# Kernel optimization log

Hardware: AMD Instinct MI355X
Metric: run time of the kernel (lower is better)

The kernel has to match this reference:

```python
import jax, jax.numpy as jnp
import numpy as np
from jax import lax

# dims: T steps, B batch, V vocab, E embed, H hidden, N cache slots, DK key dim, DV value dim
T, B, V, E, H, N, DK, DV = 64, 32, 32000, 512, 512, 512, 256, 512


def setup_inputs() -> dict:
    key = jax.random.key(0)
    ks = jax.random.split(key, 12)
    rn = lambda i, shape, scale: jax.random.normal(ks[i], shape, jnp.float32) * scale
    return {
        "tokens": jax.random.randint(ks[0], (T, B), 0, V),
        "emb": rn(1, (V, E), 0.02),
        "Wq": rn(2, (E, DK), E ** -0.5),
        "Wk": rn(3, (E, DK), E ** -0.5),
        "Wv": rn(4, (H, DV), H ** -0.5),
        "Wh": rn(5, (E + DV, H), (E + DV) ** -0.5),
        "bh": jnp.zeros((H,), jnp.float32),
        "Wout": rn(6, (H, V), H ** -0.5),
        "bout": jnp.zeros((V,), jnp.float32),
        "keys0": rn(7, (N, DK), 0.02),
        "values0": rn(8, (N, DV), 0.02),
        "k": 8,
    }


def reference(tokens, emb, Wq, Wk, Wv, Wh, bh, Wout, bout, keys0, values0, k):
    scale = 1.0 / jnp.sqrt(jnp.float32(DK))

    def step(carry, tok_t):
        keys, vals, ptr = carry
        x = emb[tok_t]                                  # [B, E] embedding gather
        q = x @ Wq                                      # [B, DK]
        scores = (q @ keys.T) * scale                   # [B, N]
        top_s, top_i = lax.top_k(scores, k)             # [B, k]
        w = jax.nn.softmax(top_s, axis=-1)              # [B, k]
        v_sel = vals[top_i]                             # [B, k, DV] irregular gather
        retrieved = jnp.einsum('bk,bkd->bd', w, v_sel)  # [B, DV]
        h = jnp.tanh(jnp.concatenate([x, retrieved], axis=-1) @ Wh + bh)  # [B, H]
        # circular-pointer cache write (batch-pooled key/value)
        new_key = jnp.mean(x @ Wk, axis=0)              # [DK]
        new_val = jnp.mean(h @ Wv, axis=0)              # [DV]
        keys = lax.dynamic_update_slice(keys, new_key[None, :], (ptr, 0))
        vals = lax.dynamic_update_slice(vals, new_val[None, :], (ptr, 0))
        ptr = (ptr + 1) % N
        return (keys, vals, ptr), h

    init = (keys0, values0, jnp.int32(0))
    _, hiddens = lax.scan(step, init, tokens)           # [T, B, H]
    logits = hiddens @ Wout + bout                      # [T, B, V]
    return logits
```

## Files before the change

kernel.cpp:

```cpp
#include <hip/hip_runtime.h>

typedef _Float16 half_t;
typedef _Float16 half8 __attribute__((ext_vector_type(8)));
typedef float f32x4 __attribute__((ext_vector_type(4)));


__device__ __forceinline__ void gload_lds16(const void* g, void* l) {
  __builtin_amdgcn_global_load_lds((const __attribute__((address_space(1))) void*)g,
                                   (__attribute__((address_space(3))) void*)l, 16, 0, 0);
}

__device__ __forceinline__ void prepTile(int pid, const float* __restrict__ Wout,
                                         half_t* __restrict__ WoutT,
                                         const float* __restrict__ Wh,
                                         half_t* __restrict__ W1T,
                                         half_t* __restrict__ W2T,
                                         char* smem) {
  half_t (*tile)[68] = (half_t(*)[68])smem;
  if (pid < 4000) {
    int n0 = (pid % 500) * 64, k0 = (pid / 500) * 64;
    for (int p = 0; p < 4; p++) {
      int id = p * 256 + threadIdx.x;
      int k = id >> 4, nq = id & 15;
      float4 v = *(const float4*)&Wout[(size_t)(k0 + k) * 32000 + n0 + nq * 4];
      tile[nq * 4 + 0][k] = (half_t)v.x; tile[nq * 4 + 1][k] = (half_t)v.y;
      tile[nq * 4 + 2][k] = (half_t)v.z; tile[nq * 4 + 3][k] = (half_t)v.w;
    }
    __syncthreads();
    for (int p = 0; p < 2; p++) {
      int id = p * 256 + threadIdx.x;
      int n = id >> 3, kc = id & 7;
      half8 h = *(const half8*)&tile[n][kc * 8];
      *(half8*)&WoutT[(size_t)(n0 + n) * 512 + k0 + kc * 8] = h;
    }
  } else {
    int id2 = pid - 4000;
    int n0 = (id2 & 7) * 64, k0 = (id2 >> 3) * 64;
    for (int p = 0; p < 16; p++) {
      int id = p * 256 + threadIdx.x;
      int kk = id >> 6, nn = id & 63;
      tile[nn][kk] = (half_t)Wh[(size_t)(k0 + kk) * 512 + n0 + nn];
    }
    __syncthreads();
    half_t* out = (k0 < 512) ? W1T : W2T;
    int kb = k0 & 511;
    for (int p = 0; p < 16; p++) {
      int id = p * 256 + threadIdx.x;
      int nn = id >> 6, kk = id & 63;
      out[(size_t)(n0 + nn) * 512 + kb + kk] = tile[nn][kk];
    }
  }
}

__global__ __launch_bounds__(256) void kGE(const int* __restrict__ tok,
                                           const float* __restrict__ emb,
                                           const float* __restrict__ Wq,
                                           const float* __restrict__ Wk,
                                           double* __restrict__ Qd,
                                           float* __restrict__ Q32,
                                           half_t* __restrict__ Xh,
                                           double* __restrict__ NKd,
                                           float* __restrict__ NKf,
                                           const float* __restrict__ Wout,
                                           half_t* __restrict__ WoutT,
                                           const float* __restrict__ Wh,
                                           half_t* __restrict__ W1T,
                                           half_t* __restrict__ W2T,
                                           int* __restrict__ DEP,
                                           int* __restrict__ bars) {
  __shared__ __align__(16) char smem[8704];
  int bid = blockIdx.x, tid = threadIdx.x;
  if (bid >= 1024) {
    if (bid < 5152) prepTile(bid - 1024, Wout, WoutT, Wh, W1T, W2T, smem);
    else { if (tid < 64) DEP[tid] = 0; bars[tid] = 0; }
    return;
  }
  if (bid < 512) {
    float (*xs)[512] = (float(*)[512])smem;
    int r0 = bid * 4;
    for (int rr = 0; rr < 4; rr++) {
      int row = r0 + rr;
      const float* src = emb + (size_t)tok[row] * 512;
      float v0 = src[tid], v1 = src[tid + 256];
      xs[rr][tid] = v0; xs[rr][tid + 256] = v1;
      Xh[(size_t)row * 512 + tid] = (half_t)v0;
      Xh[(size_t)row * 512 + tid + 256] = (half_t)v1;
    }
    __syncthreads();
    int d = tid;
    double a0 = 0, a1 = 0, a2 = 0, a3 = 0;
    #pragma unroll 4
    for (int i = 0; i < 512; i++) {
      double w = (double)Wq[(size_t)i * 256 + d];
      a0 += (double)xs[0][i] * w; a1 += (double)xs[1][i] * w;
      a2 += (double)xs[2][i] * w; a3 += (double)xs[3][i] * w;
    }
    Qd[(size_t)(r0 + 0) * 256 + d] = a0; Qd[(size_t)(r0 + 1) * 256 + d] = a1;
    Qd[(size_t)(r0 + 2) * 256 + d] = a2; Qd[(size_t)(r0 + 3) * 256 + d] = a3;
    Q32[(size_t)(r0 + 0) * 256 + d] = (float)a0; Q32[(size_t)(r0 + 1) * 256 + d] = (float)a1;
    Q32[(size_t)(r0 + 2) * 256 + d] = (float)a2; Q32[(size_t)(r0 + 3) * 256 + d] = (float)a3;
  } else {
    double* xm = (double*)smem;
    int bid2 = bid - 512, t = bid2 >> 3, ch = bid2 & 7;
    int c = tid;
    double s0 = 0.0, s1 = 0.0;
    for (int b = 0; b < 32; b++) {
      const float* src = emb + (size_t)tok[t * 32 + b] * 512;
      s0 += (double)src[c]; s1 += (double)src[c + 256];
    }
    xm[c] = s0 * (1.0 / 32.0);
    xm[c + 256] = s1 * (1.0 / 32.0);
    __syncthreads();
    if (tid < 32) {
      int d = ch * 32 + tid;
      double a = 0;
      #pragma unroll 4
      for (int i = 0; i < 512; i++) a += xm[i] * (double)Wk[(size_t)i * 256 + d];
      NKd[(size_t)t * 256 + d] = a;
      NKf[(size_t)t * 256 + d] = (float)a;
    }
  }
}

__global__ __launch_bounds__(256) void kS(const float* __restrict__ Q32,
                                          const float* __restrict__ keys0,
                                          const float* __restrict__ NKf,
                                          float* __restrict__ S) {
  __shared__ float As[32][68];
  __shared__ float Bs[32][68];
  int b = blockIdx.x, tid = threadIdx.x;
  int m0 = (b & 31) * 64, n0 = (b >> 5) * 64;
  int tx = tid & 15, ty = tid >> 4;
  float acc[4][4];
  #pragma unroll
  for (int i = 0; i < 4; i++)
    #pragma unroll
    for (int j = 0; j < 4; j++) acc[i][j] = 0.f;
  for (int kc = 0; kc < 256; kc += 32) {
    __syncthreads();
    #pragma unroll
    for (int p = 0; p < 8; p++) {
      int idx = p * 256 + tid;
      int k = idx & 31, m = idx >> 5;
      As[k][m] = Q32[(size_t)(m0 + m) * 256 + kc + k];
      int n = n0 + m;
      Bs[k][m] = (n < 512) ? keys0[(size_t)n * 256 + kc + k]
                           : NKf[(size_t)(n - 512) * 256 + kc + k];
    }
    __syncthreads();
    #pragma unroll
    for (int k = 0; k < 32; k++) {
      float4 a = *(const float4*)&As[k][ty * 4];
      float4 bb = *(const float4*)&Bs[k][tx * 4];
      acc[0][0] += a.x * bb.x; acc[0][1] += a.x * bb.y; acc[0][2] += a.x * bb.z; acc[0][3] += a.x * bb.w;
      acc[1][0] += a.y * bb.x; acc[1][1] += a.y * bb.y; acc[1][2] += a.y * bb.z; acc[1][3] += a.y * bb.w;
      acc[2][0] += a.z * bb.x; acc[2][1] += a.z * bb.y; acc[2][2] += a.z * bb.z; acc[2][3] += a.z * bb.w;
      acc[3][0] += a.w * bb.x; acc[3][1] += a.w * bb.y; acc[3][2] += a.w * bb.z; acc[3][3] += a.w * bb.w;
    }
  }
  #pragma unroll
  for (int i = 0; i < 4; i++) {
    float4 o = {acc[i][0], acc[i][1], acc[i][2], acc[i][3]};
    *(float4*)&S[(size_t)(m0 + ty * 4 + i) * 576 + n0 + tx * 4] = o;
  }
}

__global__ __launch_bounds__(256) void kTR(const float* __restrict__ S,
                                           const double* __restrict__ Qd,
                                           const double* __restrict__ NKd,
                                           const float* __restrict__ keys0,
                                           const float* __restrict__ vals0,
                                           float* __restrict__ WSo,
                                           int* __restrict__ ISo,
                                           half_t* __restrict__ R16,
                                           int* __restrict__ DEP) {
  __shared__ float wls[4][8];
  __shared__ int ils[4][8];
  __shared__ int depf;
  int bid = blockIdx.x, tid = threadIdx.x;
  if (tid == 0) depf = 0;
  __syncthreads();
  int r0b = bid * 4;
  int wv = tid >> 6, lane = tid & 63;
  int row = r0b + wv;
  int t = row >> 5;
  const float* Srow = S + (size_t)row * 576;
  float v[8];
  #pragma unroll
  for (int j = 0; j < 8; j++) v[j] = Srow[j * 64 + lane];
  if (lane < t) v[0] = Srow[512 + lane];
  int ci[12];
  #pragma unroll
  for (int it = 0; it < 12; it++) {
    float bv = -1e30f; int bi = 0x7fffffff;
    #pragma unroll
    for (int j = 0; j < 8; j++) {
      int ii = j * 64 + lane;
      if (v[j] > bv || (v[j] == bv && ii < bi)) { bv = v[j]; bi = ii; }
    }
    #pragma unroll
    for (int s = 32; s > 0; s >>= 1) {
      float ov = __shfl_xor(bv, s, 64);
      int oi = __shfl_xor(bi, s, 64);
      if (ov > bv || (ov == bv && oi < bi)) { bv = ov; bi = oi; }
    }
    ci[it] = bi;
    #pragma unroll
    for (int j = 0; j < 8; j++)
      if (j * 64 + lane == bi) v[j] = -1e30f;
  }
  const double* qrow = Qd + (size_t)row * 256 + lane * 4;
  double q0 = qrow[0], q1 = qrow[1], q2 = qrow[2], q3 = qrow[3];
  double dv[12];
  #pragma unroll
  for (int c = 0; c < 12; c++) {
    int idx = ci[c];
    double p;
    if (idx < t) {
      const double* kr = NKd + (size_t)idx * 256 + lane * 4;
      p = q0 * kr[0] + q1 * kr[1] + q2 * kr[2] + q3 * kr[3];
    } else {
      const float* kr = keys0 + (size_t)idx * 256 + lane * 4;
      p = q0 * (double)kr[0] + q1 * (double)kr[1] + q2 * (double)kr[2] + q3 * (double)kr[3];
    }
    #pragma unroll
    for (int s = 32; s > 0; s >>= 1) p += __shfl_xor(p, s, 64);
    dv[c] = p * 0.0625;
  }
  double tv[8]; int ti[8];
  #pragma unroll
  for (int it = 0; it < 8; it++) {
    double bv = -1e300; int bi = 0x7fffffff;
    #pragma unroll
    for (int c = 0; c < 12; c++)
      if (dv[c] > bv || (dv[c] == bv && ci[c] < bi)) { bv = dv[c]; bi = ci[c]; }
    tv[it] = bv; ti[it] = bi;
    #pragma unroll
    for (int c = 0; c < 12; c++)
      if (ci[c] == bi) dv[c] = -1e300;
  }
  if (lane == 0) {
    double m = tv[0], ev[8], Z = 0;
    #pragma unroll
    for (int i2 = 0; i2 < 8; i2++) { ev[i2] = exp(tv[i2] - m); Z += ev[i2]; }
    double inv = 1.0 / Z;
    int dep = 0;
    #pragma unroll
    for (int i2 = 0; i2 < 8; i2++) {
      float w = (float)(ev[i2] * inv);
      WSo[(size_t)row * 8 + i2] = w;
      ISo[(size_t)row * 8 + i2] = ti[i2];
      wls[wv][i2] = w; ils[wv][i2] = ti[i2];
      if (ti[i2] < t) dep = 1;
    }
    if (dep) atomicOr(&depf, 1);
  }
  __syncthreads();
  if (tid == 0 && depf) atomicOr(&DEP[t], 1);
  for (int rr = 0; rr < 4; rr++) {
    float a0 = 0.f, a1 = 0.f;
    #pragma unroll
    for (int k2 = 0; k2 < 8; k2++) {
      const float* src = vals0 + (size_t)ils[rr][k2] * 512;
      a0 += wls[rr][k2] * src[tid];
      a1 += wls[rr][k2] * src[tid + 256];
    }
    R16[(size_t)(r0b + rr) * 512 + tid] = (half_t)a0;
    R16[(size_t)(r0b + rr) * 512 + tid + 256] = (half_t)a1;
  }
}

__device__ __forceinline__ void gbar(int* bars, int id, int nwg) {
  __syncthreads();
  if (threadIdx.x == 0) {
    __hip_atomic_fetch_add(&bars[id], 1, __ATOMIC_ACQ_REL, __HIP_MEMORY_SCOPE_AGENT);
    while (__hip_atomic_load(&bars[id], __ATOMIC_ACQUIRE, __HIP_MEMORY_SCOPE_AGENT) < nwg)
      __builtin_amdgcn_s_sleep(4);
  }
  __syncthreads();
}

__global__ __launch_bounds__(256) void kH(const half_t* __restrict__ Xh,
                                          const half_t* __restrict__ R16,
                                          const half_t* __restrict__ W1T,
                                          const half_t* __restrict__ W2T,
                                          const float* __restrict__ bh,
                                          const float* __restrict__ Wv,
                                          float* __restrict__ XH,
                                          half_t* __restrict__ HH,
                                          float* __restrict__ HM,
                                          float* __restrict__ NV,
                                          int* __restrict__ bars) {
  __shared__ half_t lA[3][64 * 32];
  __shared__ half_t lB[3][64 * 32];
  __shared__ float hmld[512];
  int b = blockIdx.x;
  int m0 = (b >> 3) * 64, n0 = (b & 7) * 64;
  int tid = threadIdx.x, wid = tid >> 6, lane = tid & 63;
  int wm = wid >> 1, wn = wid & 1;
  f32x4 acc[2][2];
  #pragma unroll
  for (int i = 0; i < 2; i++)
    #pragma unroll
    for (int j = 0; j < 2; j++) acc[i][j] = (f32x4){0.f, 0.f, 0.f, 0.f};
  int rA = lane >> 2;
  int cswz = ((lane & 3) ^ ((lane >> 3) & 3)) * 8;
  int koffs = (((lane >> 4) ^ ((lane >> 1) & 3))) * 8;
  auto issue = [&](int j, int buf) {
    const half_t* Ap = (j < 16) ? Xh : R16;
    const half_t* Bp = (j < 16) ? W1T : W2T;
    int kk = j & 15;
    gload_lds16(Ap + ((size_t)(m0 + wid * 16 + rA) * 512 + kk * 32 + cswz), (void*)(&lA[buf][wid * 512]));
    gload_lds16(Bp + ((size_t)(n0 + wid * 16 + rA) * 512 + kk * 32 + cswz), (void*)(&lB[buf][wid * 512]));
  };
  issue(0, 0); issue(1, 1);
  for (int kt = 0; kt < 32; kt++) {
    if (kt < 31) asm volatile("s_waitcnt vmcnt(2)\n\ts_barrier" ::: "memory");
    else         asm volatile("s_waitcnt vmcnt(0)\n\ts_barrier" ::: "memory");
    int cur = kt % 3;
    half8 af[2], bf[2];
    #pragma unroll
    for (int mf = 0; mf < 2; mf++)
      af[mf] = *(const half8*)&lA[cur][(wm * 32 + mf * 16 + (lane & 15)) * 32 + koffs];
    #pragma unroll
    for (int nf = 0; nf < 2; nf++)
      bf[nf] = *(const half8*)&lB[cur][(wn * 32 + nf * 16 + (lane & 15)) * 32 + koffs];
    if (kt < 30) issue(kt + 2, (kt + 2) % 3);
    #pragma unroll
    for (int mf = 0; mf < 2; mf++)
      #pragma unroll
      for (int nf = 0; nf < 2; nf++)
        acc[mf][nf] = __builtin_amdgcn_mfma_f32_16x16x32_f16(af[mf], bf[nf], acc[mf][nf], 0, 0, 0);
    if (kt == 15) {
      #pragma unroll
      for (int nf = 0; nf < 2; nf++) {
        int col = n0 + wn * 32 + nf * 16 + (lane & 15);
        float bv = bh[col];
        #pragma unroll
        for (int mf = 0; mf < 2; mf++) {
          int rbase = m0 + wm * 32 + mf * 16 + (lane >> 4) * 4;
          #pragma unroll
          for (int r = 0; r < 4; r++)
            XH[(size_t)(rbase + r) * 512 + col] = acc[mf][nf][r] + bv;
        }
      }
    }
  }
  #pragma unroll
  for (int nf = 0; nf < 2; nf++) {
    int col = n0 + wn * 32 + nf * 16 + (lane & 15);
    float bv = bh[col];
    float cs = 0.f;
    #pragma unroll
    for (int mf = 0; mf < 2; mf++) {
      int rbase = m0 + wm * 32 + mf * 16 + (lane >> 4) * 4;
      #pragma unroll
      for (int r = 0; r < 4; r++) {
        float v = tanhf(acc[mf][nf][r] + bv);
        HH[(size_t)(rbase + r) * 512 + col] = (half_t)v;
        cs += v;
      }
    }
    cs += __shfl_xor(cs, 16, 64);
    cs += __shfl_xor(cs, 32, 64);
    if ((lane >> 4) == 0) {
      int t = (m0 >> 5) + wm;
      HM[(size_t)t * 512 + col] = cs * (1.f / 32.f);
    }
  }
  gbar(bars, 0, 256);
  int t2 = b >> 2, ch = b & 3;
  hmld[tid] = HM[(size_t)t2 * 512 + tid];
  hmld[tid + 256] = HM[(size_t)t2 * 512 + tid + 256];
  __syncthreads();
  if (tid < 128) {
    int col = ch * 128 + tid;
    float a = 0.f;
    #pragma unroll 4
    for (int i = 0; i < 512; i++) a += hmld[i] * Wv[(size_t)i * 512 + col];
    NV[(size_t)t2 * 512 + col] = a;
  }
}

__global__ __launch_bounds__(256) void kFixup(const int* __restrict__ DEP,
                                              int* __restrict__ bars,
                                              const float* __restrict__ XHm,
                                              const float* __restrict__ Wh,
                                              const float* __restrict__ Wv,
                                              const float* __restrict__ vals0,
                                              const float* __restrict__ WSo,
                                              const int* __restrict__ ISo,
                                              float* __restrict__ NV,
                                              float* __restrict__ RETR,
                                              float* __restrict__ HB,
                                              half_t* __restrict__ HHm) {
  __shared__ float rl[512];
  __shared__ float hm2[512];
  int w = blockIdx.x;
  int barid = 0;
  for (int t = 0; t < 64; t++) {
    if (DEP[t] == 0) continue;
    {
      int b = w >> 1, hf = w & 1;
      int c = hf * 256 + threadIdx.x;
      int row = t * 32 + b;
      float acc = 0.f;
      #pragma unroll
      for (int k2 = 0; k2 < 8; k2++) {
        int idx = ISo[(size_t)row * 8 + k2];
        float wv2 = WSo[(size_t)row * 8 + k2];
        const float* src = (idx < t) ? (NV + (size_t)idx * 512) : (vals0 + (size_t)idx * 512);
        acc += wv2 * src[c];
      }
      RETR[(size_t)b * 512 + c] = acc;
    }
    gbar(bars, barid++, 64);
    if (w < 32) {
      int b = w;
      rl[threadIdx.x] = RETR[(size_t)b * 512 + threadIdx.x];
      rl[threadIdx.x + 256] = RETR[(size_t)b * 512 + threadIdx.x + 256];
      __syncthreads();
      int row = t * 32 + b;
      for (int cc = 0; cc < 2; cc++) {
        int col = cc * 256 + threadIdx.x;
        float acc = 0.f;
        #pragma unroll 4
        for (int i = 0; i < 512; i++) acc += rl[i] * Wh[(size_t)(512 + i) * 512 + col];
        float h = tanhf(XHm[(size_t)row * 512 + col] + acc);
        HB[(size_t)b * 512 + col] = h;
        HHm[(size_t)row * 512 + col] = (half_t)h;
      }
    }
    gbar(bars, barid++, 64);
    if (w == 0) {
      for (int j = threadIdx.x; j < 512; j += 256) {
        float s = 0.f;
        for (int b = 0; b < 32; b++) s += HB[(size_t)b * 512 + j];
        hm2[j] = s * (1.f / 32.f);
      }
      __syncthreads();
      for (int v = threadIdx.x; v < 512; v += 256) {
        float a = 0.f;
        #pragma unroll 4
        for (int i = 0; i < 512; i++) a += hm2[i] * Wv[(size_t)i * 512 + v];
        NV[(size_t)t * 512 + v] = a;
      }
    }
    gbar(bars, barid++, 64);
  }
}

__global__ __launch_bounds__(512, 4) void kLogits(const half_t* __restrict__ A,
                                                  const half_t* __restrict__ Bm,
                                                  const float* __restrict__ bout,
                                                  float* __restrict__ C) {
  __shared__ __align__(16) char smem[49152];
  int lin = blockIdx.x;
  int g = (lin & 7) * 250 + (lin >> 3);
  int mtile = g & 15, ntile = g >> 4;
  int m0 = mtile * 128, n0 = ntile * 256;
  int tid = threadIdx.x, wid = tid >> 6, lane = tid & 63;
  int wm = wid >> 2, wn = wid & 3;
  int srow = tid >> 2, ssl = tid & 3;
  f32x4 acc[4][4];
  #pragma unroll
  for (int i = 0; i < 4; i++)
    #pragma unroll
    for (int j = 0; j < 4; j++) acc[i][j] = (f32x4){0.f, 0.f, 0.f, 0.f};
  auto issueA = [&](int kt) {
    gload_lds16(A + (size_t)(m0 + srow) * 512 + kt * 32 + ssl * 8,
                smem + (kt & 1) * 8192 + tid * 16);
  };
  auto issueB = [&](int kt) {
    #pragma unroll
    for (int j = 0; j < 2; j++)
      gload_lds16(Bm + (size_t)(n0 + j * 128 + srow) * 512 + kt * 32 + ssl * 8,
                  smem + 16384 + (kt & 1) * 16384 + j * 8192 + tid * 16);
  };
  issueA(0); issueB(0);
  for (int kt = 0; kt < 16; kt++) {
    asm volatile("s_waitcnt vmcnt(0)\n\ts_barrier" ::: "memory");
    if (kt < 15) issueA(kt + 1);
    char* Ab = smem + (kt & 1) * 8192;
    char* Bb = smem + 16384 + (kt & 1) * 16384;
    int ko = (lane >> 4) * 16;
    half8 af[4], bf[4];
    #pragma unroll
    for (int mf = 0; mf < 4; mf++)
      af[mf] = *(const half8*)(Ab + (wm * 64 + mf * 16 + (lane & 15)) * 64 + ko);
    #pragma unroll
    for (int nf = 0; nf < 4; nf++)
      bf[nf] = *(const half8*)(Bb + (wn * 64 + nf * 16 + (lane & 15)) * 64 + ko);
    __builtin_amdgcn_s_setprio(1);
    #pragma unroll
    for (int mf = 0; mf < 4; mf++)
      #pragma unroll
      for (int nf = 0; nf < 4; nf++)
        acc[mf][nf] = __builtin_amdgcn_mfma_f32_16x16x32_f16(af[mf], bf[nf], acc[mf][nf], 0, 0, 0);
    __builtin_amdgcn_s_setprio(0);
    if (kt < 15) issueB(kt + 1);
  }
  #pragma unroll
  for (int nf = 0; nf < 4; nf++) {
    int col = n0 + wn * 64 + nf * 16 + (lane & 15);
    float bv = bout[col];
    #pragma unroll
    for (int mf = 0; mf < 4; mf++) {
      int rbase = m0 + wm * 64 + mf * 16 + (lane >> 4) * 4;
      #pragma unroll
      for (int r = 0; r < 4; r++)
        C[(size_t)(rbase + r) * 32000 + col] = acc[mf][nf][r] + bv;
    }
  }
}

extern "C" void kernel_launch(void* const* d_in, const int* in_sizes, int n_in,
                              void* d_out, int out_size, void* d_ws, size_t ws_size,
                              hipStream_t stream) {
  (void)in_sizes; (void)n_in; (void)out_size; (void)ws_size;
  const int*   tok   = (const int*)d_in[0];
  const float* emb   = (const float*)d_in[1];
  const float* Wq    = (const float*)d_in[2];
  const float* Wk    = (const float*)d_in[3];
  const float* Wv    = (const float*)d_in[4];
  const float* Wh    = (const float*)d_in[5];
  const float* bh    = (const float*)d_in[6];
  const float* Wout  = (const float*)d_in[7];
  const float* bout  = (const float*)d_in[8];
  const float* keys0 = (const float*)d_in[9];
  const float* vals0 = (const float*)d_in[10];
  float* Cout = (float*)d_out;

  char* ws = (char*)d_ws;
  size_t off = 0;
  auto alloc = [&](size_t bytes) -> char* {
    char* p = ws + off;
    off += (bytes + 255) & ~(size_t)255;
    return p;
  };
  half_t* WoutT = (half_t*)alloc(32768000);
  half_t* W1T   = (half_t*)alloc(524288);
  half_t* W2T   = (half_t*)alloc(524288);
  half_t* Xh    = (half_t*)alloc(2097152);
  double* Qd    = (double*)alloc(4194304);
  float*  Q32   = (float*) alloc(2097152);
  double* NKd   = (double*)alloc(131072);
  float*  NKf   = (float*) alloc(65536);
  float*  Sb    = (float*) alloc(4718592);
  float*  XH    = (float*) alloc(4194304);
  float*  WSb   = (float*) alloc(65536);
  int*    ISb   = (int*)   alloc(65536);
  float*  NV    = (float*) alloc(131072);
  half_t* R16   = (half_t*)alloc(2097152);
  half_t* HH    = (half_t*)alloc(2097152);
  float*  HM    = (float*) alloc(131072);
  float*  RETR  = (float*) alloc(65536);
  float*  HB    = (float*) alloc(65536);
  int*    DEP   = (int*)   alloc(256);
  int*    bars  = (int*)   alloc(1024);

  kGE<<<5153, 256, 0, stream>>>(tok, emb, Wq, Wk, Qd, Q32, Xh, NKd, NKf,
                                Wout, WoutT, Wh, W1T, W2T, DEP, bars);
  kS<<<288, 256, 0, stream>>>(Q32, keys0, NKf, Sb);
  kTR<<<512, 256, 0, stream>>>(Sb, Qd, NKd, keys0, vals0, WSb, ISb, R16, DEP);
  kH<<<256, 256, 0, stream>>>(Xh, R16, W1T, W2T, bh, Wv, XH, HH, HM, NV, bars);
  kFixup<<<64, 256, 0, stream>>>(DEP, bars + 16, XH, Wh, Wv, vals0, WSb, ISb, NV, RETR, HB, HH);
  kLogits<<<2000, 512, 0, stream>>>(HH, WoutT, bout, Cout);
}
```

Baseline: 328.8 us.

## Fuse score, top-k, hidden and fixup kernels into one persistent kernel

Merges the kS, kTR, kH and kFixup launches into a single 512-workgroup persistent kernel whose stages are separated by global atomic barriers. The aim is to remove three kernel launch gaps and the tail drain between them. In exchange, every stage boundary and every fixup step now waits on a barrier across all 512 workgroups instead of 64, and the fused kernel must keep all workgroups co-resident to avoid deadlock.

```diff
diff --git a/kernel.cpp b/kernel.cpp
--- a/kernel.cpp
+++ b/kernel.cpp
@@ -122,154 +122,6 @@
   }
 }
 
-__global__ __launch_bounds__(256) void kS(const float* __restrict__ Q32,
-                                          const float* __restrict__ keys0,
-                                          const float* __restrict__ NKf,
-                                          float* __restrict__ S) {
-  __shared__ float As[32][68];
-  __shared__ float Bs[32][68];
-  int b = blockIdx.x, tid = threadIdx.x;
-  int m0 = (b & 31) * 64, n0 = (b >> 5) * 64;
-  int tx = tid & 15, ty = tid >> 4;
-  float acc[4][4];
-  #pragma unroll
-  for (int i = 0; i < 4; i++)
-    #pragma unroll
-    for (int j = 0; j < 4; j++) acc[i][j] = 0.f;
-  for (int kc = 0; kc < 256; kc += 32) {
-    __syncthreads();
-    #pragma unroll
-    for (int p = 0; p < 8; p++) {
-      int idx = p * 256 + tid;
-      int k = idx & 31, m = idx >> 5;
-      As[k][m] = Q32[(size_t)(m0 + m) * 256 + kc + k];
-      int n = n0 + m;
-      Bs[k][m] = (n < 512) ? keys0[(size_t)n * 256 + kc + k]
-                           : NKf[(size_t)(n - 512) * 256 + kc + k];
-    }
-    __syncthreads();
-    #pragma unroll
-    for (int k = 0; k < 32; k++) {
-      float4 a = *(const float4*)&As[k][ty * 4];
-      float4 bb = *(const float4*)&Bs[k][tx * 4];
-      acc[0][0] += a.x * bb.x; acc[0][1] += a.x * bb.y; acc[0][2] += a.x * bb.z; acc[0][3] += a.x * bb.w;
-      acc[1][0] += a.y * bb.x; acc[1][1] += a.y * bb.y; acc[1][2] += a.y * bb.z; acc[1][3] += a.y * bb.w;
-      acc[2][0] += a.z * bb.x; acc[2][1] += a.z * bb.y; acc[2][2] += a.z * bb.z; acc[2][3] += a.z * bb.w;
-      acc[3][0] += a.w * bb.x; acc[3][1] += a.w * bb.y; acc[3][2] += a.w * bb.z; acc[3][3] += a.w * bb.w;
-    }
-  }
-  #pragma unroll
-  for (int i = 0; i < 4; i++) {
-    float4 o = {acc[i][0], acc[i][1], acc[i][2], acc[i][3]};
-    *(float4*)&S[(size_t)(m0 + ty * 4 + i) * 576 + n0 + tx * 4] = o;
-  }
-}
-
-__global__ __launch_bounds__(256) void kTR(const float* __restrict__ S,
-                                           const double* __restrict__ Qd,
-                                           const double* __restrict__ NKd,
-                                           const float* __restrict__ keys0,
-                                           const float* __restrict__ vals0,
-                                           float* __restrict__ WSo,
-                                           int* __restrict__ ISo,
-                                           half_t* __restrict__ R16,
-                                           int* __restrict__ DEP) {
-  __shared__ float wls[4][8];
-  __shared__ int ils[4][8];
-  __shared__ int depf;
-  int bid = blockIdx.x, tid = threadIdx.x;
-  if (tid == 0) depf = 0;
-  __syncthreads();
-  int r0b = bid * 4;
-  int wv = tid >> 6, lane = tid & 63;
-  int row = r0b + wv;
-  int t = row >> 5;
-  const float* Srow = S + (size_t)row * 576;
-  float v[8];
-  #pragma unroll
-  for (int j = 0; j < 8; j++) v[j] = Srow[j * 64 + lane];
-  if (lane < t) v[0] = Srow[512 + lane];
-  int ci[12];
-  #pragma unroll
-  for (int it = 0; it < 12; it++) {
-    float bv = -1e30f; int bi = 0x7fffffff;
-    #pragma unroll
-    for (int j = 0; j < 8; j++) {
-      int ii = j * 64 + lane;
-      if (v[j] > bv || (v[j] == bv && ii < bi)) { bv = v[j]; bi = ii; }
-    }
-    #pragma unroll
-    for (int s = 32; s > 0; s >>= 1) {
-      float ov = __shfl_xor(bv, s, 64);
-      int oi = __shfl_xor(bi, s, 64);
-      if (ov > bv || (ov == bv && oi < bi)) { bv = ov; bi = oi; }
-    }
-    ci[it] = bi;
-    #pragma unroll
-    for (int j = 0; j < 8; j++)
-      if (j * 64 + lane == bi) v[j] = -1e30f;
-  }
-  const double* qrow = Qd + (size_t)row * 256 + lane * 4;
-  double q0 = qrow[0], q1 = qrow[1], q2 = qrow[2], q3 = qrow[3];
-  double dv[12];
-  #pragma unroll
-  for (int c = 0; c < 12; c++) {
-    int idx = ci[c];
-    double p;
-    if (idx < t) {
-      const double* kr = NKd + (size_t)idx * 256 + lane * 4;
-      p = q0 * kr[0] + q1 * kr[1] + q2 * kr[2] + q3 * kr[3];
-    } else {
-      const float* kr = keys0 + (size_t)idx * 256 + lane * 4;
-      p = q0 * (double)kr[0] + q1 * (double)kr[1] + q2 * (double)kr[2] + q3 * (double)kr[3];
-    }
-    #pragma unroll
-    for (int s = 32; s > 0; s >>= 1) p += __shfl_xor(p, s, 64);
-    dv[c] = p * 0.0625;
-  }
-  double tv[8]; int ti[8];
-  #pragma unroll
-  for (int it = 0; it < 8; it++) {
-    double bv = -1e300; int bi = 0x7fffffff;
-    #pragma unroll
-    for (int c = 0; c < 12; c++)
-      if (dv[c] > bv || (dv[c] == bv && ci[c] < bi)) { bv = dv[c]; bi = ci[c]; }
-    tv[it] = bv; ti[it] = bi;
-    #pragma unroll
-    for (int c = 0; c < 12; c++)
-      if (ci[c] == bi) dv[c] = -1e300;
-  }
-  if (lane == 0) {
-    double m = tv[0], ev[8], Z = 0;
-    #pragma unroll
-    for (int i2 = 0; i2 < 8; i2++) { ev[i2] = exp(tv[i2] - m); Z += ev[i2]; }
-    double inv = 1.0 / Z;
-    int dep = 0;
-    #pragma unroll
-    for (int i2 = 0; i2 < 8; i2++) {
-      float w = (float)(ev[i2] * inv);
-      WSo[(size_t)row * 8 + i2] = w;
-      ISo[(size_t)row * 8 + i2] = ti[i2];
-      wls[wv][i2] = w; ils[wv][i2] = ti[i2];
-      if (ti[i2] < t) dep = 1;
-    }
-    if (dep) atomicOr(&depf, 1);
-  }
-  __syncthreads();
-  if (tid == 0 && depf) atomicOr(&DEP[t], 1);
-  for (int rr = 0; rr < 4; rr++) {
-    float a0 = 0.f, a1 = 0.f;
-    #pragma unroll
-    for (int k2 = 0; k2 < 8; k2++) {
-      const float* src = vals0 + (size_t)ils[rr][k2] * 512;
-      a0 += wls[rr][k2] * src[tid];
-      a1 += wls[rr][k2] * src[tid + 256];
-    }
-    R16[(size_t)(r0b + rr) * 512 + tid] = (half_t)a0;
-    R16[(size_t)(r0b + rr) * 512 + tid + 256] = (half_t)a1;
-  }
-}
-
 __device__ __forceinline__ void gbar(int* bars, int id, int nwg) {
   __syncthreads();
   if (threadIdx.x == 0) {
@@ -280,129 +132,264 @@
   __syncthreads();
 }
 
-__global__ __launch_bounds__(256) void kH(const half_t* __restrict__ Xh,
-                                          const half_t* __restrict__ R16,
-                                          const half_t* __restrict__ W1T,
-                                          const half_t* __restrict__ W2T,
-                                          const float* __restrict__ bh,
-                                          const float* __restrict__ Wv,
-                                          float* __restrict__ XH,
-                                          half_t* __restrict__ HH,
-                                          float* __restrict__ HM,
-                                          float* __restrict__ NV,
-                                          int* __restrict__ bars) {
-  __shared__ half_t lA[3][64 * 32];
-  __shared__ half_t lB[3][64 * 32];
-  __shared__ float hmld[512];
-  int b = blockIdx.x;
-  int m0 = (b >> 3) * 64, n0 = (b & 7) * 64;
-  int tid = threadIdx.x, wid = tid >> 6, lane = tid & 63;
-  int wm = wid >> 1, wn = wid & 1;
-  f32x4 acc[2][2];
-  #pragma unroll
-  for (int i = 0; i < 2; i++)
-    #pragma unroll
-    for (int j = 0; j < 2; j++) acc[i][j] = (f32x4){0.f, 0.f, 0.f, 0.f};
-  int rA = lane >> 2;
-  int cswz = ((lane & 3) ^ ((lane >> 3) & 3)) * 8;
-  int koffs = (((lane >> 4) ^ ((lane >> 1) & 3))) * 8;
-  auto issue = [&](int j, int buf) {
-    const half_t* Ap = (j < 16) ? Xh : R16;
-    const half_t* Bp = (j < 16) ? W1T : W2T;
-    int kk = j & 15;
-    gload_lds16(Ap + ((size_t)(m0 + wid * 16 + rA) * 512 + kk * 32 + cswz), (void*)(&lA[buf][wid * 512]));
-    gload_lds16(Bp + ((size_t)(n0 + wid * 16 + rA) * 512 + kk * 32 + cswz), (void*)(&lB[buf][wid * 512]));
-  };
-  issue(0, 0); issue(1, 1);
-  for (int kt = 0; kt < 32; kt++) {
-    if (kt < 31) asm volatile("s_waitcnt vmcnt(2)\n\ts_barrier" ::: "memory");
-    else         asm volatile("s_waitcnt vmcnt(0)\n\ts_barrier" ::: "memory");
-    int cur = kt % 3;
-    half8 af[2], bf[2];
-    #pragma unroll
-    for (int mf = 0; mf < 2; mf++)
-      af[mf] = *(const half8*)&lA[cur][(wm * 32 + mf * 16 + (lane & 15)) * 32 + koffs];
-    #pragma unroll
-    for (int nf = 0; nf < 2; nf++)
-      bf[nf] = *(const half8*)&lB[cur][(wn * 32 + nf * 16 + (lane & 15)) * 32 + koffs];
-    if (kt < 30) issue(kt + 2, (kt + 2) % 3);
-    #pragma unroll
-    for (int mf = 0; mf < 2; mf++)
+__global__ __launch_bounds__(256) void kBig(
+    const float* __restrict__ Q32, const float* __restrict__ keys0,
+    const float* __restrict__ NKf, float* __restrict__ Sb,
+    const double* __restrict__ Qd, const double* __restrict__ NKd,
+    const float* __restrict__ vals0,
+    float* __restrict__ WSo, int* __restrict__ ISo, half_t* __restrict__ R16,
+    int* __restrict__ DEP, int* __restrict__ bars,
+    const half_t* __restrict__ Xh, const half_t* __restrict__ W1T,
+    const half_t* __restrict__ W2T, const float* __restrict__ bh,
+    const float* __restrict__ Wv, const float* __restrict__ Wh,
+    float* __restrict__ XH, half_t* __restrict__ HH, float* __restrict__ HM,
+    float* __restrict__ NV, float* __restrict__ RETR, float* __restrict__ HB) {
+  __shared__ __align__(16) char smem[26624];
+  __shared__ float wls[4][8];
+  __shared__ int ils[4][8];
+  __shared__ int depf;
+  __shared__ int depl[64];
+  int w = blockIdx.x, tid = threadIdx.x;
+
+  if (w < 288) {
+    float (*As)[68] = (float(*)[68])smem;
+    float (*Bs)[68] = (float(*)[68])(smem + 8704);
+    int m0 = (w & 31) * 64, n0 = (w >> 5) * 64;
+    int tx = tid & 15, ty = tid >> 4;
+    float acc[4][4];
+    #pragma unroll
+    for (int i = 0; i < 4; i++)
+      #pragma unroll
+      for (int j = 0; j < 4; j++) acc[i][j] = 0.f;
+    for (int kc = 0; kc < 256; kc += 32) {
+      __syncthreads();
+      #pragma unroll
+      for (int p = 0; p < 8; p++) {
+        int idx = p * 256 + tid;
+        int k = idx & 31, m = idx >> 5;
+        As[k][m] = Q32[(size_t)(m0 + m) * 256 + kc + k];
+        int n = n0 + m;
+        Bs[k][m] = (n < 512) ? keys0[(size_t)n * 256 + kc + k]
+                             : NKf[(size_t)(n - 512) * 256 + kc + k];
+      }
+      __syncthreads();
+      #pragma unroll
+      for (int k = 0; k < 32; k++) {
+        float4 a = *(const float4*)&As[k][ty * 4];
+        float4 bb = *(const float4*)&Bs[k][tx * 4];
+        acc[0][0] += a.x * bb.x; acc[0][1] += a.x * bb.y; acc[0][2] += a.x * bb.z; acc[0][3] += a.x * bb.w;
+        acc[1][0] += a.y * bb.x; acc[1][1] += a.y * bb.y; acc[1][2] += a.y * bb.z; acc[1][3] += a.y * bb.w;
+        acc[2][0] += a.z * bb.x; acc[2][1] += a.z * bb.y; acc[2][2] += a.z * bb.z; acc[2][3] += a.z * bb.w;
+        acc[3][0] += a.w * bb.x; acc[3][1] += a.w * bb.y; acc[3][2] += a.w * bb.z; acc[3][3] += a.w * bb.w;
+      }
+    }
+    #pragma unroll
+    for (int i = 0; i < 4; i++) {
+      float4 o = {acc[i][0], acc[i][1], acc[i][2], acc[i][3]};
+      *(float4*)&Sb[(size_t)(m0 + ty * 4 + i) * 576 + n0 + tx * 4] = o;
+    }
+  }
+  gbar(bars, 0, 512);
+
+  {
+    if (tid == 0) depf = 0;
+    __syncthreads();
+    int r0b = w * 4;
+    int wv = tid >> 6, lane = tid & 63;
+    int row = r0b + wv;
+    int t = row >> 5;
+    const float* Srow = Sb + (size_t)row * 576;
+    float v[8];
+    #pragma unroll
+    for (int j = 0; j < 8; j++) v[j] = Srow[j * 64 + lane];
+    if (lane < t) v[0] = Srow[512 + lane];
+    int ci[12];
+    #pragma unroll
+    for (int it = 0; it < 12; it++) {
+      float bv = -1e30f; int bi = 0x7fffffff;
+      #pragma unroll
+      for (int j = 0; j < 8; j++) {
+        int ii = j * 64 + lane;
+        if (v[j] > bv || (v[j] == bv && ii < bi)) { bv = v[j]; bi = ii; }
+      }
+      #pragma unroll
+      for (int s = 32; s > 0; s >>= 1) {
+        float ov = __shfl_xor(bv, s, 64);
+        int oi = __shfl_xor(bi, s, 64);
+        if (ov > bv || (ov == bv && oi < bi)) { bv = ov; bi = oi; }
+      }
+      ci[it] = bi;
+      #pragma unroll
+      for (int j = 0; j < 8; j++)
+        if (j * 64 + lane == bi) v[j] = -1e30f;
+    }
+    const double* qrow = Qd + (size_t)row * 256 + lane * 4;
+    double q0 = qrow[0], q1 = qrow[1], q2 = qrow[2], q3 = qrow[3];
+    double dv[12];
+    #pragma unroll
+    for (int c = 0; c < 12; c++) {
+      int idx = ci[c];
+      double p;
+      if (idx < t) {
+        const double* kr = NKd + (size_t)idx * 256 + lane * 4;
+        p = q0 * kr[0] + q1 * kr[1] + q2 * kr[2] + q3 * kr[3];
+      } else {
+        const float* kr = keys0 + (size_t)idx * 256 + lane * 4;
+        p = q0 * (double)kr[0] + q1 * (double)kr[1] + q2 * (double)kr[2] + q3 * (double)kr[3];
+      }
+      #pragma unroll
+      for (int s = 32; s > 0; s >>= 1) p += __shfl_xor(p, s, 64);
+      dv[c] = p * 0.0625;
+    }
+    double tv[8]; int ti[8];
+    #pragma unroll
+    for (int it = 0; it < 8; it++) {
+      double bv = -1e300; int bi = 0x7fffffff;
+      #pragma unroll
+      for (int c = 0; c < 12; c++)
+        if (dv[c] > bv || (dv[c] == bv && ci[c] < bi)) { bv = dv[c]; bi = ci[c]; }
+      tv[it] = bv; ti[it] = bi;
+      #pragma unroll
+      for (int c = 0; c < 12; c++)
+        if (ci[c] == bi) dv[c] = -1e300;
+    }
+    if (lane == 0) {
+      double m = tv[0], ev[8], Z = 0;
+      #pragma unroll
+      for (int i2 = 0; i2 < 8; i2++) { ev[i2] = exp(tv[i2] - m); Z += ev[i2]; }
+      double inv = 1.0 / Z;
+      int dep = 0;
+      #pragma unroll
+      for (int i2 = 0; i2 < 8; i2++) {
+        float wgt = (float)(ev[i2] * inv);
+        WSo[(size_t)row * 8 + i2] = wgt;
+        ISo[(size_t)row * 8 + i2] = ti[i2];
+        wls[wv][i2] = wgt; ils[wv][i2] = ti[i2];
+        if (ti[i2] < t) dep = 1;
+      }
+      if (dep) atomicOr(&depf, 1);
+    }
+    __syncthreads();
+    if (tid == 0 && depf) atomicOr(&DEP[t], 1);
+    for (int rr = 0; rr < 4; rr++) {
+      float a0 = 0.f, a1 = 0.f;
+      #pragma unroll
+      for (int k2 = 0; k2 < 8; k2++) {
+        const float* src = vals0 + (size_t)ils[rr][k2] * 512;
+        a0 += wls[rr][k2] * src[tid];
+        a1 += wls[rr][k2] * src[tid + 256];
+      }
+      R16[(size_t)(r0b + rr) * 512 + tid] = (half_t)a0;
+      R16[(size_t)(r0b + rr) * 512 + tid + 256] = (half_t)a1;
+    }
+  }
+  gbar(bars, 1, 512);
+
+  if (w < 256) {
+    half_t* lAb = (half_t*)smem;
+    half_t* lBb = (half_t*)(smem + 12288);
+    int m0 = (w >> 3) * 64, n0 = (w & 7) * 64;
+    int wid = tid >> 6, lane = tid & 63;
+    int wm = wid >> 1, wn = wid & 1;
+    f32x4 acc[2][2];
+    #pragma unroll
+    for (int i = 0; i < 2; i++)
+      #pragma unroll
+      for (int j = 0; j < 2; j++) acc[i][j] = (f32x4){0.f, 0.f, 0.f, 0.f};
+    int rA = lane >> 2;
+    int cswz = ((lane & 3) ^ ((lane >> 3) & 3)) * 8;
+    int koffs = (((lane >> 4) ^ ((lane >> 1) & 3))) * 8;
+    auto issue = [&](int j, int buf) {
+      const half_t* Ap = (j < 16) ? Xh : R16;
+      const half_t* Bp = (j < 16) ? W1T : W2T;
+      int kk = j & 15;
+      gload_lds16(Ap + ((size_t)(m0 + wid * 16 + rA) * 512 + kk * 32 + cswz), (void*)(lAb + buf * 2048 + wid * 512));
+      gload_lds16(Bp + ((size_t)(n0 + wid * 16 + rA) * 512 + kk * 32 + cswz), (void*)(lBb + buf * 2048 + wid * 512));
+    };
+    issue(0, 0); issue(1, 1);
+    for (int kt = 0; kt < 32; kt++) {
+      if (kt < 31) asm volatile("s_waitcnt vmcnt(2)\n\ts_barrier" ::: "memory");
+      else         asm volatile("s_waitcnt vmcnt(0)\n\ts_barrier" ::: "memory");
+      int cur = kt % 3;
+      half8 af[2], bf[2];
+      #pragma unroll
+      for (int mf = 0; mf < 2; mf++)
+        af[mf] = *(const half8*)(lAb + cur * 2048 + (wm * 32 + mf * 16 + (lane & 15)) * 32 + koffs);
       #pragma unroll
       for (int nf = 0; nf < 2; nf++)
-        acc[mf][nf] = __builtin_amdgcn_mfma_f32_16x16x32_f16(af[mf], bf[nf], acc[mf][nf], 0, 0, 0);
-    if (kt == 15) {
-      #pragma unroll
-      for (int nf = 0; nf < 2; nf++) {
-        int col = n0 + wn * 32 + nf * 16 + (lane & 15);
-        float bv = bh[col];
+        bf[nf] = *(const half8*)(lBb + cur * 2048 + (wn * 32 + nf * 16 + (lane & 15)) * 32 + koffs);
+      if (kt < 30) issue(kt + 2, (kt + 2) % 3);
+      #pragma unroll
+      for (int mf = 0; mf < 2; mf++)
         #pragma unroll
-        for (int mf = 0; mf < 2; mf++) {
-          int rbase = m0 + wm * 32 + mf * 16 + (lane >> 4) * 4;
+        for (int nf = 0; nf < 2; nf++)
+          acc[mf][nf] = __builtin_amdgcn_mfma_f32_16x16x32_f16(af[mf], bf[nf], acc[mf][nf], 0, 0, 0);
+      if (kt == 15) {
+        #pragma unroll
+        for (int nf = 0; nf < 2; nf++) {
+          int col = n0 + wn * 32 + nf * 16 + (lane & 15);
+          float bv = bh[col];
           #pragma unroll
-          for (int r = 0; r < 4; r++)
-            XH[(size_t)(rbase + r) * 512 + col] = acc[mf][nf][r] + bv;
+          for (int mf = 0; mf < 2; mf++) {
+            int rbase = m0 + wm * 32 + mf * 16 + (lane >> 4) * 4;
+            #pragma unroll
+            for (int r = 0; r < 4; r++)
+              XH[(size_t)(rbase + r) * 512 + col] = acc[mf][nf][r] + bv;
+          }
         }
       }
     }
-  }
-  #pragma unroll
-  for (int nf = 0; nf < 2; nf++) {
-    int col = n0 + wn * 32 + nf * 16 + (lane & 15);
-    float bv = bh[col];
-    float cs = 0.f;
-    #pragma unroll
-    for (int mf = 0; mf < 2; mf++) {
-      int rbase = m0 + wm * 32 + mf * 16 + (lane >> 4) * 4;
-      #pragma unroll
-      for (int r = 0; r < 4; r++) {
-        float v = tanhf(acc[mf][nf][r] + bv);
-        HH[(size_t)(rbase + r) * 512 + col] = (half_t)v;
-        cs += v;
-      }
-    }
-    cs += __shfl_xor(cs, 16, 64);
-    cs += __shfl_xor(cs, 32, 64);
-    if ((lane >> 4) == 0) {
-      int t = (m0 >> 5) + wm;
-      HM[(size_t)t * 512 + col] = cs * (1.f / 32.f);
-    }
-  }
-  gbar(bars, 0, 256);
-  int t2 = b >> 2, ch = b & 3;
-  hmld[tid] = HM[(size_t)t2 * 512 + tid];
-  hmld[tid + 256] = HM[(size_t)t2 * 512 + tid + 256];
+    #pragma unroll
+    for (int nf = 0; nf < 2; nf++) {
+      int col = n0 + wn * 32 + nf * 16 + (lane & 15);
+      float bv = bh[col];
+      float cs = 0.f;
+      #pragma unroll
+      for (int mf = 0; mf < 2; mf++) {
+        int rbase = m0 + wm * 32 + mf * 16 + (lane >> 4) * 4;
+        #pragma unroll
+        for (int r = 0; r < 4; r++) {
+          float vv = tanhf(acc[mf][nf][r] + bv);
+          HH[(size_t)(rbase + r) * 512 + col] = (half_t)vv;
+          cs += vv;
+        }
+      }
+      cs += __shfl_xor(cs, 16, 64);
+      cs += __shfl_xor(cs, 32, 64);
+      if ((lane >> 4) == 0) {
+        int t = (m0 >> 5) + wm;
+        HM[(size_t)t * 512 + col] = cs * (1.f / 32.f);
+      }
+    }
+  }
+  gbar(bars, 2, 512);
+
+  {
+    float* hmld = (float*)smem;
+    int t2 = w >> 3, ch = w & 7;
+    hmld[tid] = HM[(size_t)t2 * 512 + tid];
+    hmld[tid + 256] = HM[(size_t)t2 * 512 + tid + 256];
+    __syncthreads();
+    if (tid < 64) {
+      int col = ch * 64 + tid;
+      float a = 0.f;
+      #pragma unroll 4
+      for (int i = 0; i < 512; i++) a += hmld[i] * Wv[(size_t)i * 512 + col];
+      NV[(size_t)t2 * 512 + col] = a;
+    }
+  }
+  gbar(bars, 3, 512);
+
+  if (tid < 64) depl[tid] = DEP[tid];
   __syncthreads();
-  if (tid < 128) {
-    int col = ch * 128 + tid;
-    float a = 0.f;
-    #pragma unroll 4
-    for (int i = 0; i < 512; i++) a += hmld[i] * Wv[(size_t)i * 512 + col];
-    NV[(size_t)t2 * 512 + col] = a;
-  }
-}
-
-__global__ __launch_bounds__(256) void kFixup(const int* __restrict__ DEP,
-                                              int* __restrict__ bars,
-                                              const float* __restrict__ XHm,
-                                              const float* __restrict__ Wh,
-                                              const float* __restrict__ Wv,
-                                              const float* __restrict__ vals0,
-                                              const float* __restrict__ WSo,
-                                              const int* __restrict__ ISo,
-                                              float* __restrict__ NV,
-                                              float* __restrict__ RETR,
-                                              float* __restrict__ HB,
-                                              half_t* __restrict__ HHm) {
-  __shared__ float rl[512];
-  __shared__ float hm2[512];
-  int w = blockIdx.x;
-  int barid = 0;
+  float* rl = (float*)smem;
+  float* hm2 = (float*)(smem + 2048);
+  int barid = 4;
   for (int t = 0; t < 64; t++) {
-    if (DEP[t] == 0) continue;
-    {
+    if (depl[t] == 0) continue;
+    if (w < 64) {
       int b = w >> 1, hf = w & 1;
-      int c = hf * 256 + threadIdx.x;
+      int c = hf * 256 + tid;
       int row = t * 32 + b;
       float acc = 0.f;
       #pragma unroll
@@ -414,39 +401,39 @@
       }
       RETR[(size_t)b * 512 + c] = acc;
     }
-    gbar(bars, barid++, 64);
+    gbar(bars, barid++, 512);
     if (w < 32) {
       int b = w;
-      rl[threadIdx.x] = RETR[(size_t)b * 512 + threadIdx.x];
-      rl[threadIdx.x + 256] = RETR[(size_t)b * 512 + threadIdx.x + 256];
+      rl[tid] = RETR[(size_t)b * 512 + tid];
+      rl[tid + 256] = RETR[(size_t)b * 512 + tid + 256];
       __syncthreads();
       int row = t * 32 + b;
       for (int cc = 0; cc < 2; cc++) {
-        int col = cc * 256 + threadIdx.x;
+        int col = cc * 256 + tid;
         float acc = 0.f;
         #pragma unroll 4
         for (int i = 0; i < 512; i++) acc += rl[i] * Wh[(size_t)(512 + i) * 512 + col];
-        float h = tanhf(XHm[(size_t)row * 512 + col] + acc);
+        float h = tanhf(XH[(size_t)row * 512 + col] + acc);
         HB[(size_t)b * 512 + col] = h;
-        HHm[(size_t)row * 512 + col] = (half_t)h;
-      }
-    }
-    gbar(bars, barid++, 64);
+        HH[(size_t)row * 512 + col] = (half_t)h;
+      }
+    }
+    gbar(bars, barid++, 512);
     if (w == 0) {
-      for (int j = threadIdx.x; j < 512; j += 256) {
+      for (int j = tid; j < 512; j += 256) {
         float s = 0.f;
         for (int b = 0; b < 32; b++) s += HB[(size_t)b * 512 + j];
         hm2[j] = s * (1.f / 32.f);
       }
       __syncthreads();
-      for (int v = threadIdx.x; v < 512; v += 256) {
+      for (int v2 = tid; v2 < 512; v2 += 256) {
         float a = 0.f;
         #pragma unroll 4
-        for (int i = 0; i < 512; i++) a += hm2[i] * Wv[(size_t)i * 512 + v];
-        NV[(size_t)t * 512 + v] = a;
-      }
-    }
-    gbar(bars, barid++, 64);
+        for (int i = 0; i < 512; i++) a += hm2[i] * Wv[(size_t)i * 512 + v2];
+        NV[(size_t)t * 512 + v2] = a;
+      }
+    }
+    gbar(bars, barid++, 512);
   }
 }
 
@@ -561,9 +548,9 @@
 
   kGE<<<5153, 256, 0, stream>>>(tok, emb, Wq, Wk, Qd, Q32, Xh, NKd, NKf,
                                 Wout, WoutT, Wh, W1T, W2T, DEP, bars);
-  kS<<<288, 256, 0, stream>>>(Q32, keys0, NKf, Sb);
-  kTR<<<512, 256, 0, stream>>>(Sb, Qd, NKd, keys0, vals0, WSb, ISb, R16, DEP);
-  kH<<<256, 256, 0, stream>>>(Xh, R16, W1T, W2T, bh, Wv, XH, HH, HM, NV, bars);
-  kFixup<<<64, 256, 0, stream>>>(DEP, bars + 16, XH, Wh, Wv, vals0, WSb, ISb, NV, RETR, HB, HH);
+  kBig<<<512, 256, 0, stream>>>(Q32, keys0, NKf, Sb, Qd, NKd, vals0,
+                                WSb, ISb, R16, DEP, bars,
+                                Xh, W1T, W2T, bh, Wv, Wh,
+                                XH, HH, HM, NV, RETR, HB);
   kLogits<<<2000, 512, 0, stream>>>(HH, WoutT, bout, Cout);
 }
```

Result: slower. 522.8 us (+59.0%).

## Fuse fixup loop into hidden kernel and cut per-step grid barriers

Applied to the files above, without the earlier changes.

Merges the sequential fixup kernel into the hidden-state GEMM kernel, which removes one launch and hands data over through the existing grid barrier. Each step now needs two barriers instead of three: every block recomputes its batch row's retrieval into LDS locally instead of writing RETR and syncing. The Wv projection for the new cache value is spread across all 64 blocks with a wave reduction instead of running on one block. In exchange the retrieval gather is done twice per batch row, and the fused kernel relies on all 256 blocks being co-resident for its barriers.

```diff
diff --git a/kernel.cpp b/kernel.cpp
--- a/kernel.cpp
+++ b/kernel.cpp
@@ -280,22 +280,30 @@
   __syncthreads();
 }
 
-__global__ __launch_bounds__(256) void kH(const half_t* __restrict__ Xh,
-                                          const half_t* __restrict__ R16,
-                                          const half_t* __restrict__ W1T,
-                                          const half_t* __restrict__ W2T,
-                                          const float* __restrict__ bh,
-                                          const float* __restrict__ Wv,
-                                          float* __restrict__ XH,
-                                          half_t* __restrict__ HH,
-                                          float* __restrict__ HM,
-                                          float* __restrict__ NV,
-                                          int* __restrict__ bars) {
+__global__ __launch_bounds__(256) void kH2(const half_t* __restrict__ Xh,
+                                           const half_t* __restrict__ R16,
+                                           const half_t* __restrict__ W1T,
+                                           const half_t* __restrict__ W2T,
+                                           const float* __restrict__ bh,
+                                           const float* __restrict__ Wv,
+                                           const float* __restrict__ Wh,
+                                           const float* __restrict__ vals0,
+                                           const float* __restrict__ WSo,
+                                           const int* __restrict__ ISo,
+                                           const int* __restrict__ DEP,
+                                           float* __restrict__ XH,
+                                           half_t* __restrict__ HH,
+                                           float* __restrict__ HM,
+                                           float* __restrict__ NV,
+                                           float* __restrict__ HB,
+                                           int* __restrict__ bars) {
   __shared__ half_t lA[3][64 * 32];
   __shared__ half_t lB[3][64 * 32];
   __shared__ float hmld[512];
-  int b = blockIdx.x;
-  int m0 = (b >> 3) * 64, n0 = (b & 7) * 64;
+  __shared__ float rl[512];
+  __shared__ int depl[64];
+  int w = blockIdx.x;
+  int m0 = (w >> 3) * 64, n0 = (w & 7) * 64;
   int tid = threadIdx.x, wid = tid >> 6, lane = tid & 63;
   int wm = wid >> 1, wn = wid & 1;
   f32x4 acc[2][2];
@@ -356,9 +364,9 @@
       int rbase = m0 + wm * 32 + mf * 16 + (lane >> 4) * 4;
       #pragma unroll
       for (int r = 0; r < 4; r++) {
-        float v = tanhf(acc[mf][nf][r] + bv);
-        HH[(size_t)(rbase + r) * 512 + col] = (half_t)v;
-        cs += v;
+        float vv = tanhf(acc[mf][nf][r] + bv);
+        HH[(size_t)(rbase + r) * 512 + col] = (half_t)vv;
+        cs += vv;
       }
     }
     cs += __shfl_xor(cs, 16, 64);
@@ -369,82 +377,67 @@
     }
   }
   gbar(bars, 0, 256);
-  int t2 = b >> 2, ch = b & 3;
-  hmld[tid] = HM[(size_t)t2 * 512 + tid];
-  hmld[tid + 256] = HM[(size_t)t2 * 512 + tid + 256];
+  {
+    int t2 = w >> 2, ch = w & 3;
+    hmld[tid] = HM[(size_t)t2 * 512 + tid];
+    hmld[tid + 256] = HM[(size_t)t2 * 512 + tid + 256];
+    __syncthreads();
+    if (tid < 128) {
+      int col = ch * 128 + tid;
+      float a = 0.f;
+      #pragma unroll 4
+      for (int i = 0; i < 512; i++) a += hmld[i] * Wv[(size_t)i * 512 + col];
+      NV[(size_t)t2 * 512 + col] = a;
+    }
+  }
+  gbar(bars, 1, 256);
+  if (w >= 64) return;
+  if (tid < 64) depl[tid] = DEP[tid];
   __syncthreads();
-  if (tid < 128) {
-    int col = ch * 128 + tid;
-    float a = 0.f;
-    #pragma unroll 4
-    for (int i = 0; i < 512; i++) a += hmld[i] * Wv[(size_t)i * 512 + col];
-    NV[(size_t)t2 * 512 + col] = a;
-  }
-}
-
-__global__ __launch_bounds__(256) void kFixup(const int* __restrict__ DEP,
-                                              int* __restrict__ bars,
-                                              const float* __restrict__ XHm,
-                                              const float* __restrict__ Wh,
-                                              const float* __restrict__ Wv,
-                                              const float* __restrict__ vals0,
-                                              const float* __restrict__ WSo,
-                                              const int* __restrict__ ISo,
-                                              float* __restrict__ NV,
-                                              float* __restrict__ RETR,
-                                              float* __restrict__ HB,
-                                              half_t* __restrict__ HHm) {
-  __shared__ float rl[512];
-  __shared__ float hm2[512];
-  int w = blockIdx.x;
-  int barid = 0;
+  int b = w >> 1, hf = w & 1;
+  int barid = 2;
   for (int t = 0; t < 64; t++) {
-    if (DEP[t] == 0) continue;
+    if (depl[t] == 0) continue;
     {
-      int b = w >> 1, hf = w & 1;
-      int c = hf * 256 + threadIdx.x;
       int row = t * 32 + b;
-      float acc = 0.f;
-      #pragma unroll
-      for (int k2 = 0; k2 < 8; k2++) {
-        int idx = ISo[(size_t)row * 8 + k2];
-        float wv2 = WSo[(size_t)row * 8 + k2];
-        const float* src = (idx < t) ? (NV + (size_t)idx * 512) : (vals0 + (size_t)idx * 512);
-        acc += wv2 * src[c];
-      }
-      RETR[(size_t)b * 512 + c] = acc;
-    }
-    gbar(bars, barid++, 64);
-    if (w < 32) {
-      int b = w;
-      rl[threadIdx.x] = RETR[(size_t)b * 512 + threadIdx.x];
-      rl[threadIdx.x + 256] = RETR[(size_t)b * 512 + threadIdx.x + 256];
-      __syncthreads();
-      int row = t * 32 + b;
-      for (int cc = 0; cc < 2; cc++) {
-        int col = cc * 256 + threadIdx.x;
-        float acc = 0.f;
-        #pragma unroll 4
-        for (int i = 0; i < 512; i++) acc += rl[i] * Wh[(size_t)(512 + i) * 512 + col];
-        float h = tanhf(XHm[(size_t)row * 512 + col] + acc);
-        HB[(size_t)b * 512 + col] = h;
-        HHm[(size_t)row * 512 + col] = (half_t)h;
-      }
-    }
-    gbar(bars, barid++, 64);
-    if (w == 0) {
-      for (int j = threadIdx.x; j < 512; j += 256) {
-        float s = 0.f;
-        for (int b = 0; b < 32; b++) s += HB[(size_t)b * 512 + j];
-        hm2[j] = s * (1.f / 32.f);
+      for (int c = tid; c < 512; c += 256) {
+        float a = 0.f;
+        #pragma unroll
+        for (int k2 = 0; k2 < 8; k2++) {
+          int idx = ISo[(size_t)row * 8 + k2];
+          float wv2 = WSo[(size_t)row * 8 + k2];
+          const float* src = (idx < t) ? (NV + (size_t)idx * 512) : (vals0 + (size_t)idx * 512);
+          a += wv2 * src[c];
+        }
+        rl[c] = a;
       }
       __syncthreads();
-      for (int v = threadIdx.x; v < 512; v += 256) {
-        float a = 0.f;
-        #pragma unroll 4
-        for (int i = 0; i < 512; i++) a += hm2[i] * Wv[(size_t)i * 512 + v];
-        NV[(size_t)t * 512 + v] = a;
+      int col = hf * 256 + tid;
+      float a = 0.f;
+      #pragma unroll 4
+      for (int i = 0; i < 512; i++) a += rl[i] * Wh[(size_t)(512 + i) * 512 + col];
+      float h = tanhf(XH[(size_t)row * 512 + col] + a);
+      HB[(size_t)b * 512 + col] = h;
+      HH[(size_t)row * 512 + col] = (half_t)h;
+    }
+    gbar(bars, barid++, 64);
+    {
+      float s0 = 0.f, s1 = 0.f;
+      for (int bb = 0; bb < 32; bb++) {
+        s0 += HB[(size_t)bb * 512 + tid];
+        s1 += HB[(size_t)bb * 512 + tid + 256];
       }
+      hmld[tid] = s0 * (1.f / 32.f);
+      hmld[tid + 256] = s1 * (1.f / 32.f);
+      __syncthreads();
+      int g = wid * 2 + ((lane >> 5) & 1);
+      int l32 = lane & 31;
+      int col = w * 8 + g;
+      float a = 0.f;
+      for (int i = l32; i < 512; i += 32) a += hmld[i] * Wv[(size_t)i * 512 + col];
+      #pragma unroll
+      for (int s = 16; s > 0; s >>= 1) a += __shfl_xor(a, s, 64);
+      if (l32 == 0) NV[(size_t)t * 512 + col] = a;
     }
     gbar(bars, barid++, 64);
   }
@@ -554,7 +547,6 @@
   half_t* R16   = (half_t*)alloc(2097152);
   half_t* HH    = (half_t*)alloc(2097152);
   float*  HM    = (float*) alloc(131072);
-  float*  RETR  = (float*) alloc(65536);
   float*  HB    = (float*) alloc(65536);
   int*    DEP   = (int*)   alloc(256);
   int*    bars  = (int*)   alloc(1024);
@@ -563,7 +555,7 @@
                                 Wout, WoutT, Wh, W1T, W2T, DEP, bars);
   kS<<<288, 256, 0, stream>>>(Q32, keys0, NKf, Sb);
   kTR<<<512, 256, 0, stream>>>(Sb, Qd, NKd, keys0, vals0, WSb, ISb, R16, DEP);
-  kH<<<256, 256, 0, stream>>>(Xh, R16, W1T, W2T, bh, Wv, XH, HH, HM, NV, bars);
-  kFixup<<<64, 256, 0, stream>>>(DEP, bars + 16, XH, Wh, Wv, vals0, WSb, ISb, NV, RETR, HB, HH);
+  kH2<<<256, 256, 0, stream>>>(Xh, R16, W1T, W2T, bh, Wv, Wh, vals0,
+                               WSb, ISb, DEP, XH, HH, HM, NV, HB, bars);
   kLogits<<<2000, 512, 0, stream>>>(HH, WoutT, bout, Cout);
 }
```

Result: no change. 330.6 us (+0.5%).
